# Optimization experiments

Hardware: AMD Instinct MI355X
Metric: run time of the kernel (lower is better)

The kernel has to match this reference:

```python
import math
import jax, jax.numpy as jnp
import numpy as np

D_MODEL = 1024
NUM_HEADS = 16
HEAD_DIM = D_MODEL // NUM_HEADS
B, T = 2, 2048


def setup_inputs() -> dict:
    key = jax.random.key(0)
    ks = jax.random.split(key, 11)
    s = 0.02
    inp = {
        'x':  jax.random.normal(ks[0], (B, T, D_MODEL), dtype=jnp.float32),
        'Wq': jax.random.normal(ks[1], (D_MODEL, D_MODEL), dtype=jnp.float32) * s,
        'bq': jax.random.normal(ks[2], (D_MODEL,), dtype=jnp.float32) * s,
        'Wk': jax.random.normal(ks[3], (D_MODEL, D_MODEL), dtype=jnp.float32) * s,
        'bk': jax.random.normal(ks[4], (D_MODEL,), dtype=jnp.float32) * s,
        'Wv': jax.random.normal(ks[5], (D_MODEL, D_MODEL), dtype=jnp.float32) * s,
        'bv': jax.random.normal(ks[6], (D_MODEL,), dtype=jnp.float32) * s,
        'Wt': jax.random.normal(ks[7], (D_MODEL, D_MODEL), dtype=jnp.float32) * s,
        'bt': jax.random.normal(ks[8], (D_MODEL,), dtype=jnp.float32) * s,
        'Wo': jax.random.normal(ks[9], (D_MODEL, D_MODEL), dtype=jnp.float32) * s,
        'bo': jax.random.normal(ks[10], (D_MODEL,), dtype=jnp.float32) * s,
    }
    return inp


def reference(x, Wq, bq, Wk, bk, Wv, bv, Wt, bt, Wo, bo):
    Bx, Tx, D = x.shape
    H, hd = NUM_HEADS, HEAD_DIM
    scale = 1.0 / math.sqrt(hd)

    def proj(W, b):
        # (B,T,D) -> (B,H,T,hd); torch Linear uses x @ W.T + b
        return (x @ W.T + b).reshape(Bx, Tx, H, hd).transpose(0, 2, 1, 3)

    q = proj(Wq, bq)
    k = proj(Wk, bk)
    v = proj(Wv, bv)
    t = proj(Wt, bt)

    # dot-product term: (B,H,T,T)
    scores = jnp.einsum('bhqd,bhkd->bhqk', q, k)
    # triplet term: cumsum over key positions of (k*v)/sqrt(hd)
    kv_cumsum = jnp.cumsum(k * v * scale, axis=2)  # (B,H,T,hd)
    scores = scores + jnp.einsum('bhqd,bhkd->bhqk', q * t, kv_cumsum)
    scores = scores * scale

    # causal mask: position j > i forbidden
    causal = jnp.tril(jnp.ones((Tx, Tx), dtype=bool))
    scores = jnp.where(causal[None, None], scores, jnp.float32(-jnp.inf))

    attn = jax.nn.softmax(scores, axis=-1)  # stable max-subtract internally
    out = jnp.einsum('bhqk,bhkd->bhqd', attn, v)
    out = out.transpose(0, 2, 1, 3).reshape(Bx, Tx, D)
    return out @ Wo.T + bo
```

## Files before the change

### kernel.cpp

```cpp
#include <hip/hip_runtime.h>
#include <hip/hip_bf16.h>

typedef unsigned short u16;
typedef __attribute__((ext_vector_type(8))) short bf16x8;
typedef __attribute__((ext_vector_type(4))) float f32x4;
typedef __attribute__((ext_vector_type(4))) unsigned int u32x4;

#define LOG2E 1.44269504088896340736f

static __device__ __forceinline__ float b2f(u16 u) {
    union { float f; unsigned int i; } v; v.i = ((unsigned int)u) << 16; return v.f;
}
static __device__ __forceinline__ u16 f2b(float f) {
    unsigned int x = __builtin_bit_cast(unsigned int, f);
    unsigned int r = (x + 0x7fffu + ((x >> 16) & 1u)) >> 16;
    return (u16)r;
}
static __device__ __forceinline__ void gll16(const u16* g, u16* l) {
    __builtin_amdgcn_global_load_lds((const __attribute__((address_space(1))) void*)g,
                                     (__attribute__((address_space(3))) void*)l, 16, 0, 0);
}
static __device__ __forceinline__ float fexp2(float x) {
    float r; asm("v_exp_f32 %0, %1" : "=v"(r) : "v"(x)); return r;
}

__global__ __launch_bounds__(256) void cvt_all(const float* __restrict__ x,
                                               const float* __restrict__ w0, const float* __restrict__ w1,
                                               const float* __restrict__ w2, const float* __restrict__ w3,
                                               const float* __restrict__ w4, u16* __restrict__ dst) {
    size_t c = (size_t)blockIdx.x * 256 + threadIdx.x;
    size_t e = c * 4;
    const float* s; size_t off;
    const size_t M4 = (size_t)4 << 20, M1 = (size_t)1 << 20;
    if (e < M4) { s = x; off = e; }
    else {
        size_t r = e - M4; int wsel = (int)(r >> 20); off = r & (M1 - 1);
        s = wsel == 0 ? w0 : wsel == 1 ? w1 : wsel == 2 ? w2 : wsel == 3 ? w3 : w4;
    }
    float4 v = *(const float4*)(s + off);
    u16* d = dst + e;
    d[0] = f2b(v.x); d[1] = f2b(v.y); d[2] = f2b(v.z); d[3] = f2b(v.w);
}

template<int WM>
static __device__ __forceinline__ void gemm_body(const u16* __restrict__ A, const u16* __restrict__ W,
                                                 const float* __restrict__ bias, void* __restrict__ outp,
                                                 int mode, u16* Al, u16* Bl) {
    const int tid = threadIdx.x, lane = tid & 63, w = tid >> 6;
    const int wr = w >> 1, wc = w & 1;
    const int l15 = lane & 15, lhi = lane >> 4;
    const int tm = blockIdx.y * (WM * 32), tn = blockIdx.x * 128;

    f32x4 acc[WM][4] = {};

    for (int kt = 0; kt < 16; ++kt) {
        const int k0 = kt * 64;
        #pragma unroll
        for (int i = 0; i < WM; ++i) {
            int rl = i * 32 + w * 8 + (lane >> 3);
            int c  = (lane & 7) ^ (rl & 7);
            gll16(A + (size_t)(tm + rl) * 1024 + k0 + c * 8, Al + (i * 32 + w * 8) * 64);
        }
        #pragma unroll
        for (int i = 0; i < 4; ++i) {
            int rl = i * 32 + w * 8 + (lane >> 3);
            int c  = (lane & 7) ^ (rl & 7);
            gll16(W + (size_t)(tn + rl) * 1024 + k0 + c * 8, Bl + (i * 32 + w * 8) * 64);
        }
        __syncthreads();
        #pragma unroll
        for (int ks = 0; ks < 2; ++ks) {
            bf16x8 af[WM], bfr[4];
            #pragma unroll
            for (int mi = 0; mi < WM; ++mi) {
                int row = wr * (WM * 16) + mi * 16 + l15;
                int cc = (ks * 4 + lhi) ^ (row & 7);
                af[mi] = *(const bf16x8*)(Al + row * 64 + cc * 8);
            }
            #pragma unroll
            for (int ni = 0; ni < 4; ++ni) {
                int row = wc * 64 + ni * 16 + l15;
                int cc = (ks * 4 + lhi) ^ (row & 7);
                bfr[ni] = *(const bf16x8*)(Bl + row * 64 + cc * 8);
            }
            #pragma unroll
            for (int mi = 0; mi < WM; ++mi)
                #pragma unroll
                for (int ni = 0; ni < 4; ++ni)
                    acc[mi][ni] = __builtin_amdgcn_mfma_f32_16x16x32_bf16(af[mi], bfr[ni], acc[mi][ni], 0, 0, 0);
        }
        __syncthreads();
    }

    float bcol[4];
    #pragma unroll
    for (int ni = 0; ni < 4; ++ni) bcol[ni] = bias[tn + wc * 64 + ni * 16 + l15];

    #pragma unroll
    for (int mi = 0; mi < WM; ++mi)
        #pragma unroll
        for (int ni = 0; ni < 4; ++ni)
            #pragma unroll
            for (int r = 0; r < 4; ++r) {
                int rg = tm + wr * (WM * 16) + mi * 16 + lhi * 4 + r;
                int cg = tn + wc * 64 + ni * 16 + l15;
                float v = acc[mi][ni][r] + bcol[ni];
                if (mode == 2) {
                    ((float*)outp)[(size_t)rg * 1024 + cg] = v;
                } else {
                    int b = rg >> 11, t = rg & 2047, h = cg >> 6, d = cg & 63;
                    if (mode == 0)
                        ((u16*)outp)[(((size_t)(b * 16 + h)) * 2048 + t) * 128 + d] = f2b(v);
                    else
                        ((u16*)outp)[(((size_t)(b * 16 + h)) * 2048 + t) * 64 + d] = f2b(v);
                }
            }
}

struct ProjArgs {
    const u16* W[4];
    const float* b[4];
    u16* out[4];
};

__global__ __launch_bounds__(256) void gemm_proj(const u16* __restrict__ A, ProjArgs pa) {
    __shared__ u16 Al[128 * 64];
    __shared__ u16 Bl[128 * 64];
    const int z = blockIdx.z;
    gemm_body<4>(A, pa.W[z], pa.b[z], pa.out[z], (z < 2) ? 0 : 1, Al, Bl);
}

__global__ __launch_bounds__(256) void gemm_out2(const u16* __restrict__ A, const u16* __restrict__ W,
                                                 const float* __restrict__ bias, void* __restrict__ out) {
    __shared__ u16 Al[64 * 64];
    __shared__ u16 Bl[128 * 64];
    gemm_body<2>(A, W, bias, out, 2, Al, Bl);
}

__global__ __launch_bounds__(256) void fuse_small(u16* __restrict__ Qa, const u16* __restrict__ Tp,
                                                  const u16* __restrict__ V, u16* __restrict__ VT,
                                                  u16* __restrict__ Ka) {
    __shared__ char shmem[64 * 72 * 2];
    const int b = blockIdx.x, tid = threadIdx.x;

    if (b < 2048) {
        int idx = b * 256 + tid;
        int tg = idx >> 3, dc = idx & 7;
        bf16x8 q = *(const bf16x8*)(Qa + (size_t)tg * 128 + dc * 8);
        bf16x8 tt = *(const bf16x8*)(Tp + (size_t)tg * 64 + dc * 8);
        bf16x8 o;
        #pragma unroll
        for (int j = 0; j < 8; ++j) o[j] = (short)f2b(b2f((u16)q[j]) * b2f((u16)tt[j]));
        *(bf16x8*)(Qa + (size_t)tg * 128 + 64 + dc * 8) = o;
    } else if (b < 3072) {
        u16 (*tile)[72] = (u16(*)[72])shmem;
        const int r0 = b - 2048;
        const int bh = r0 >> 5, tc = r0 & 31;
        const u16* Vh = V + ((size_t)bh * 2048 + tc * 64) * 64;
        u16* VTh = VT + (size_t)bh * 64 * 2048 + tc * 64;
        for (int i = 0; i < 2; ++i) {
            int f = i * 256 + tid;
            int r = f >> 3, dc = f & 7;
            bf16x8 v = *(const bf16x8*)(Vh + r * 64 + dc * 8);
            #pragma unroll
            for (int j = 0; j < 8; ++j) tile[dc * 8 + j][r] = (u16)v[j];
        }
        __syncthreads();
        for (int i = 0; i < 2; ++i) {
            int f = i * 256 + tid;
            int d = f >> 3, t8 = (f & 7) * 8;
            bf16x8 o;
            #pragma unroll
            for (int j = 0; j < 8; ++j) {
                int pos = t8 + j;
                int key = (pos & 32) + 16 * ((pos >> 2) & 1) + 4 * ((pos >> 3) & 3) + (pos & 3);
                o[j] = (short)tile[d][key];
            }
            *(bf16x8*)(VTh + (size_t)d * 2048 + t8) = o;
        }
    } else {
        float4* sums = (float4*)shmem;
        const int r0 = b - 3072;
        const int bh = r0 & 31, dg = r0 >> 5;
        u16* Kh = Ka + (size_t)bh * 2048 * 128;
        const u16* Vh = V + (size_t)bh * 2048 * 64;
        const int quad = tid & 3, c = tid >> 2;
        const int d0 = dg * 16 + quad * 4;
        float s0 = 0.f, s1 = 0.f, s2 = 0.f, s3 = 0.f;
        for (int i = 0; i < 32; ++i) {
            int t = c * 32 + i;
            ushort4 kv = *(const ushort4*)(Kh + (size_t)t * 128 + d0);
            ushort4 vv = *(const ushort4*)(Vh + (size_t)t * 64 + d0);
            s0 += b2f(kv.x) * b2f(vv.x);
            s1 += b2f(kv.y) * b2f(vv.y);
            s2 += b2f(kv.z) * b2f(vv.z);
            s3 += b2f(kv.w) * b2f(vv.w);
        }
        float4 sv; sv.x = s0; sv.y = s1; sv.z = s2; sv.w = s3;
        sums[c * 4 + quad] = sv;
        __syncthreads();
        float4 run; run.x = run.y = run.z = run.w = 0.f;
        for (int cc = 0; cc < c; ++cc) {
            float4 ss = sums[cc * 4 + quad];
            run.x += ss.x; run.y += ss.y; run.z += ss.z; run.w += ss.w;
        }
        for (int i = 0; i < 32; ++i) {
            int t = c * 32 + i;
            ushort4 kv = *(const ushort4*)(Kh + (size_t)t * 128 + d0);
            ushort4 vv = *(const ushort4*)(Vh + (size_t)t * 64 + d0);
            run.x += b2f(kv.x) * b2f(vv.x);
            run.y += b2f(kv.y) * b2f(vv.y);
            run.z += b2f(kv.z) * b2f(vv.z);
            run.w += b2f(kv.w) * b2f(vv.w);
            ushort4 o;
            o.x = f2b(run.x * 0.125f); o.y = f2b(run.y * 0.125f);
            o.z = f2b(run.z * 0.125f); o.w = f2b(run.w * 0.125f);
            *(ushort4*)(Kh + (size_t)t * 128 + 64 + d0) = o;
        }
    }
}

__global__ __launch_bounds__(256, 3) void attn5(const u16* __restrict__ Qa, const u16* __restrict__ Ka,
                                                const u16* __restrict__ VT, u16* __restrict__ Obuf) {
    const int wg = blockIdx.x;
    const int xcd = wg & 7, slot = wg >> 3;
    const int bh = xcd * 4 + (slot >> 4);
    const int qp = slot & 15;
    const int tiL = qp, tiH = 31 - qp;
    const int q0L = tiL * 64, q0H = tiH * 64;
    const int NT = tiH + 1;
    const u16* Qh = Qa + (size_t)bh * 2048 * 128;
    const u16* Kh = Ka + (size_t)bh * 2048 * 128;
    const u16* VTh = VT + (size_t)bh * 64 * 2048;

    __shared__ u16 Kl[2][64 * 128];
    __shared__ u16 Vl[2][64 * 64];

    const int tid = threadIdx.x, lane = tid & 63, w = tid >> 6;
    const int l15 = lane & 15, lhi = lane >> 4;
    const float SC = 0.125f * LOG2E;

    bf16x8 qfL[4], qfH[4];
    #pragma unroll
    for (int ks = 0; ks < 4; ++ks) {
        bf16x8 a = *(const bf16x8*)(Qh + (size_t)(q0L + w * 16 + l15) * 128 + ks * 32 + lhi * 8);
        bf16x8 b = *(const bf16x8*)(Qh + (size_t)(q0H + w * 16 + l15) * 128 + ks * 32 + lhi * 8);
        bf16x8 oa, ob;
        #pragma unroll
        for (int j = 0; j < 8; ++j) {
            oa[j] = (short)f2b(b2f((u16)a[j]) * SC);
            ob[j] = (short)f2b(b2f((u16)b[j]) * SC);
        }
        qfL[ks] = oa; qfH[ks] = ob;
    }

    f32x4 accL[4] = {}, accH[4] = {};
    float lsL = 0.f, lsH = 0.f;

    auto STAGE = [&](int buf, int ti) {
        const int kv0 = ti * 64;
        #pragma unroll
        for (int i = 0; i < 4; ++i) {
            int lr = i * 16 + w * 4 + lhi;
            int c = l15 ^ (lr & 15);
            gll16(Kh + (size_t)(kv0 + lr) * 128 + c * 8, &Kl[buf][(i * 16 + w * 4) * 128]);
        }
        #pragma unroll
        for (int i = 0; i < 2; ++i) {
            int dr = i * 32 + w * 8 + (lane >> 3);
            int c = (lane & 7) ^ (dr & 7);
            gll16(VTh + (size_t)dr * 2048 + kv0 + c * 8, &Vl[buf][(i * 32 + w * 8) * 64]);
        }
    };

    STAGE(0, 0);
    asm volatile("s_waitcnt vmcnt(0)" ::: "memory");
    __builtin_amdgcn_s_barrier();

    for (int ti = 0; ti < NT; ++ti) {
        const int cur = ti & 1;
        if (ti + 1 < NT) STAGE(cur ^ 1, ti + 1);
        const bool doL = (ti <= tiL);

        f32x4 sH[4] = {}, sL[4] = {};
        #pragma unroll
        for (int ks = 0; ks < 4; ++ks) {
            bf16x8 kf[4];
            #pragma unroll
            for (int k2 = 0; k2 < 4; ++k2) {
                int kl = k2 * 16 + l15;
                int cc = (ks * 4 + lhi) ^ l15;
                kf[k2] = *(const bf16x8*)(&Kl[cur][kl * 128 + cc * 8]);
            }
            __builtin_amdgcn_s_setprio(1);
            #pragma unroll
            for (int k2 = 0; k2 < 4; ++k2)
                sH[k2] = __builtin_amdgcn_mfma_f32_16x16x32_bf16(kf[k2], qfH[ks], sH[k2], 0, 0, 0);
            if (doL) {
                #pragma unroll
                for (int k2 = 0; k2 < 4; ++k2)
                    sL[k2] = __builtin_amdgcn_mfma_f32_16x16x32_bf16(kf[k2], qfL[ks], sL[k2], 0, 0, 0);
            }
            __builtin_amdgcn_s_setprio(0);
        }

        auto FINISH = [&](f32x4* sacc, f32x4* acc, float& lsum, bool diag) {
            float p[4][4];
            #pragma unroll
            for (int k2 = 0; k2 < 4; ++k2)
                #pragma unroll
                for (int r = 0; r < 4; ++r) {
                    float s = sacc[k2][r];
                    if (diag) {
                        int key = k2 * 16 + lhi * 4 + r;
                        int qq = w * 16 + l15;
                        s = (key <= qq) ? s : -1e30f;
                    }
                    float pe = fexp2(s);
                    p[k2][r] = pe;
                    lsum += pe;
                }
            bf16x8 pf[2];
            #pragma unroll
            for (int ks2 = 0; ks2 < 2; ++ks2) {
                unsigned int w0, w1, w2, w3;
                asm("v_cvt_pk_bf16_f32 %0, %1, %2" : "=v"(w0) : "v"(p[2 * ks2][0]),     "v"(p[2 * ks2][1]));
                asm("v_cvt_pk_bf16_f32 %0, %1, %2" : "=v"(w1) : "v"(p[2 * ks2][2]),     "v"(p[2 * ks2][3]));
                asm("v_cvt_pk_bf16_f32 %0, %1, %2" : "=v"(w2) : "v"(p[2 * ks2 + 1][0]), "v"(p[2 * ks2 + 1][1]));
                asm("v_cvt_pk_bf16_f32 %0, %1, %2" : "=v"(w3) : "v"(p[2 * ks2 + 1][2]), "v"(p[2 * ks2 + 1][3]));
                u32x4 t = {w0, w1, w2, w3};
                pf[ks2] = __builtin_bit_cast(bf16x8, t);
            }
            #pragma unroll
            for (int ks2 = 0; ks2 < 2; ++ks2) {
                __builtin_amdgcn_s_setprio(1);
                #pragma unroll
                for (int dt = 0; dt < 4; ++dt) {
                    int dd = dt * 16 + l15;
                    int cc = (ks2 * 4 + lhi) ^ (dd & 7);
                    bf16x8 vf = *(const bf16x8*)(&Vl[cur][dd * 64 + cc * 8]);
                    acc[dt] = __builtin_amdgcn_mfma_f32_16x16x32_bf16(pf[ks2], vf, acc[dt], 0, 0, 0);
                }
                __builtin_amdgcn_s_setprio(0);
            }
        };

        FINISH(sH, accH, lsH, ti == tiH);
        if (doL) FINISH(sL, accL, lsL, ti == tiL);

        asm volatile("s_waitcnt vmcnt(0)" ::: "memory");
        __builtin_amdgcn_s_barrier();
    }

    lsH += __shfl_xor(lsH, 16, 64); lsH += __shfl_xor(lsH, 32, 64);
    lsL += __shfl_xor(lsL, 16, 64); lsL += __shfl_xor(lsL, 32, 64);
    float invH[4], invL[4];
    #pragma unroll
    for (int r = 0; r < 4; ++r) {
        invH[r] = 1.0f / __shfl(lsH, lhi * 4 + r, 64);
        invL[r] = 1.0f / __shfl(lsL, lhi * 4 + r, 64);
    }
    #pragma unroll
    for (int dt = 0; dt < 4; ++dt)
        #pragma unroll
        for (int r = 0; r < 4; ++r) {
            int cr = lhi * 4 + r;
            int dd = dt * 16 + l15;
            int qgL = q0L + w * 16 + cr;
            int qgH = q0H + w * 16 + cr;
            size_t nL = (size_t)(bh >> 4) * 2048 + qgL;
            size_t nH = (size_t)(bh >> 4) * 2048 + qgH;
            Obuf[nL * 1024 + (bh & 15) * 64 + dd] = f2b(accL[dt][r] * invL[r]);
            Obuf[nH * 1024 + (bh & 15) * 64 + dd] = f2b(accH[dt][r] * invH[r]);
        }
}

extern "C" void kernel_launch(void* const* d_in, const int* in_sizes, int n_in,
                              void* d_out, int out_size, void* d_ws, size_t ws_size,
                              hipStream_t stream) {
    (void)in_sizes; (void)n_in; (void)out_size; (void)ws_size;
    const float* x  = (const float*)d_in[0];
    const float* Wq = (const float*)d_in[1];
    const float* bq = (const float*)d_in[2];
    const float* Wk = (const float*)d_in[3];
    const float* bk = (const float*)d_in[4];
    const float* Wv = (const float*)d_in[5];
    const float* bv = (const float*)d_in[6];
    const float* Wt = (const float*)d_in[7];
    const float* bt = (const float*)d_in[8];
    const float* Wo = (const float*)d_in[9];
    const float* bo = (const float*)d_in[10];

    const size_t M1 = 1024u * 1024u;
    u16* xb   = (u16*)d_ws;
    u16* wq   = xb + 4 * M1;
    u16* wk   = wq + M1;
    u16* wv   = wk + M1;
    u16* wt   = wv + M1;
    u16* wo   = wt + M1;
    u16* Qa   = wo + M1;
    u16* Kaa  = Qa + 8 * M1;
    u16* Vtm  = Kaa + 8 * M1;
    u16* Ttm  = Vtm + 4 * M1;
    u16* Obuf = Ttm + 4 * M1;
    u16* VTg  = xb;

    cvt_all<<<9216, 256, 0, stream>>>(x, Wq, Wk, Wv, Wt, Wo, xb);

    ProjArgs pa;
    pa.W[0] = wq; pa.W[1] = wk; pa.W[2] = wv; pa.W[3] = wt;
    pa.b[0] = bq; pa.b[1] = bk; pa.b[2] = bv; pa.b[3] = bt;
    pa.out[0] = Qa; pa.out[1] = Kaa; pa.out[2] = Vtm; pa.out[3] = Ttm;
    gemm_proj<<<dim3(8, 32, 4), 256, 0, stream>>>(xb, pa);

    fuse_small<<<3200, 256, 0, stream>>>(Qa, Ttm, Vtm, VTg, Kaa);

    attn5<<<512, 256, 0, stream>>>(Qa, Kaa, VTg, Obuf);

    gemm_out2<<<dim3(8, 64), 256, 0, stream>>>(Obuf, wo, bo, d_out);
}
```

Before: 145.7 us.

## Share A tile across two projection weights per block in QKVT GEMM

The projection GEMM now computes two output projections per block (Q with K, V with T), so each A tile loaded into LDS is reused for two B tiles. This halves the number of A-tile loads and halves the grid along z. In exchange each block uses twice the accumulators (128 floats per lane) and more LDS, which lowers occupancy and may cause register pressure, and the grid shrinks from 1024 to 512 blocks.

```diff
diff --git a/kernel.cpp b/kernel.cpp
--- a/kernel.cpp
+++ b/kernel.cpp
@@ -123,11 +123,84 @@
     u16* out[4];
 };
 
-__global__ __launch_bounds__(256) void gemm_proj(const u16* __restrict__ A, ProjArgs pa) {
+__global__ __launch_bounds__(256) void gemm_proj2(const u16* __restrict__ A, ProjArgs pa) {
     __shared__ u16 Al[128 * 64];
-    __shared__ u16 Bl[128 * 64];
+    __shared__ u16 Bl[2][128 * 64];
     const int z = blockIdx.z;
-    gemm_body<4>(A, pa.W[z], pa.b[z], pa.out[z], (z < 2) ? 0 : 1, Al, Bl);
+    const u16* W0 = pa.W[z * 2];
+    const u16* W1 = pa.W[z * 2 + 1];
+
+    const int tid = threadIdx.x, lane = tid & 63, w = tid >> 6;
+    const int wr = w >> 1, wc = w & 1;
+    const int l15 = lane & 15, lhi = lane >> 4;
+    const int tm = blockIdx.y * 128, tn = blockIdx.x * 128;
+
+    f32x4 acc[2][4][4] = {};
+
+    for (int kt = 0; kt < 16; ++kt) {
+        const int k0 = kt * 64;
+        #pragma unroll
+        for (int i = 0; i < 4; ++i) {
+            int rl = i * 32 + w * 8 + (lane >> 3);
+            int c  = (lane & 7) ^ (rl & 7);
+            gll16(A  + (size_t)(tm + rl) * 1024 + k0 + c * 8, Al    + (i * 32 + w * 8) * 64);
+            gll16(W0 + (size_t)(tn + rl) * 1024 + k0 + c * 8, Bl[0] + (i * 32 + w * 8) * 64);
+            gll16(W1 + (size_t)(tn + rl) * 1024 + k0 + c * 8, Bl[1] + (i * 32 + w * 8) * 64);
+        }
+        __syncthreads();
+        #pragma unroll
+        for (int ks = 0; ks < 2; ++ks) {
+            bf16x8 af[4];
+            #pragma unroll
+            for (int mi = 0; mi < 4; ++mi) {
+                int row = wr * 64 + mi * 16 + l15;
+                int cc = (ks * 4 + lhi) ^ (row & 7);
+                af[mi] = *(const bf16x8*)(Al + row * 64 + cc * 8);
+            }
+            #pragma unroll
+            for (int zz = 0; zz < 2; ++zz) {
+                bf16x8 bfr[4];
+                #pragma unroll
+                for (int ni = 0; ni < 4; ++ni) {
+                    int row = wc * 64 + ni * 16 + l15;
+                    int cc = (ks * 4 + lhi) ^ (row & 7);
+                    bfr[ni] = *(const bf16x8*)(&Bl[zz][row * 64 + cc * 8]);
+                }
+                __builtin_amdgcn_s_setprio(1);
+                #pragma unroll
+                for (int mi = 0; mi < 4; ++mi)
+                    #pragma unroll
+                    for (int ni = 0; ni < 4; ++ni)
+                        acc[zz][mi][ni] = __builtin_amdgcn_mfma_f32_16x16x32_bf16(af[mi], bfr[ni], acc[zz][mi][ni], 0, 0, 0);
+                __builtin_amdgcn_s_setprio(0);
+            }
+        }
+        __syncthreads();
+    }
+
+    #pragma unroll
+    for (int zz = 0; zz < 2; ++zz) {
+        const float* bias = pa.b[z * 2 + zz];
+        u16* outp = pa.out[z * 2 + zz];
+        float bcol[4];
+        #pragma unroll
+        for (int ni = 0; ni < 4; ++ni) bcol[ni] = bias[tn + wc * 64 + ni * 16 + l15];
+        #pragma unroll
+        for (int mi = 0; mi < 4; ++mi)
+            #pragma unroll
+            for (int ni = 0; ni < 4; ++ni)
+                #pragma unroll
+                for (int r = 0; r < 4; ++r) {
+                    int rg = tm + wr * 64 + mi * 16 + lhi * 4 + r;
+                    int cg = tn + wc * 64 + ni * 16 + l15;
+                    float v = acc[zz][mi][ni][r] + bcol[ni];
+                    int b = rg >> 11, t = rg & 2047, h = cg >> 6, d = cg & 63;
+                    if (z == 0)
+                        outp[(((size_t)(b * 16 + h)) * 2048 + t) * 128 + d] = f2b(v);
+                    else
+                        outp[(((size_t)(b * 16 + h)) * 2048 + t) * 64 + d] = f2b(v);
+                }
+    }
 }
 
 __global__ __launch_bounds__(256) void gemm_out2(const u16* __restrict__ A, const u16* __restrict__ W,
@@ -411,7 +484,7 @@
     pa.W[0] = wq; pa.W[1] = wk; pa.W[2] = wv; pa.W[3] = wt;
     pa.b[0] = bq; pa.b[1] = bk; pa.b[2] = bv; pa.b[3] = bt;
     pa.out[0] = Qa; pa.out[1] = Kaa; pa.out[2] = Vtm; pa.out[3] = Ttm;
-    gemm_proj<<<dim3(8, 32, 4), 256, 0, stream>>>(xb, pa);
+    gemm_proj2<<<dim3(8, 32, 2), 256, 0, stream>>>(xb, pa);
 
     fuse_small<<<3200, 256, 0, stream>>>(Qa, Ttm, Vtm, VTg, Kaa);
 
```

New measurement: 165.7 us. +13.7%, slower.
